# Optimization experiments

Hardware: AMD Instinct MI355X
Metric: run time of the kernel (lower is better)

Reference implementation:

```python
import jax, jax.numpy as jnp
import numpy as np

N_CLASSES = 4096
FEAT_DIM = 2048


def setup_inputs() -> dict:
    key = jax.random.key(0)
    k1, k2, k3 = jax.random.split(key, 3)
    boundaries = jax.random.uniform(k1, (N_CLASSES,), dtype=jnp.float32)
    prototypes = jax.random.normal(k2, (N_CLASSES, FEAT_DIM), dtype=jnp.float32)
    classifier_weights = jax.random.normal(k3, (N_CLASSES, FEAT_DIM), dtype=jnp.float32)
    return {"boundaries": boundaries, "prototypes": prototypes,
            "classifier_weights": classifier_weights}


def reference(boundaries, prototypes, classifier_weights):
    n = boundaries.shape[0]
    # L2-normalize prototypes along feature dim (F.normalize, eps=1e-12)
    norm = jnp.sqrt(jnp.sum(prototypes * prototypes, axis=-1, keepdims=True))
    p = prototypes / jnp.maximum(norm, 1e-12)
    # s[i, j] = <p_i, w_j>  -- one GEMM instead of N^2 tiny dots
    s = p @ classifier_weights.T  # [N, N]
    diag = jnp.diagonal(s)  # <p_i, w_i>, shape [N]
    # term1 depends only on i, term2 on (i, j)
    term1 = (1.0 - boundaries) * diag  # [N]
    term2 = s * (boundaries - 1.0)[None, :]  # [N, N], broadcast over j
    vals = jax.nn.relu(term1[:, None] + term2)  # [N, N]
    # exclude i == j
    off_diag_sum = jnp.sum(vals) - jnp.sum(jnp.diagonal(vals))
    return off_diag_sum / (n * (n - 1))
```

## Files before the change

kernel.cpp:

```cpp
#include <hip/hip_runtime.h>
#include <hip/hip_bf16.h>

#define N_CLS 4096
#define FDIM  2048
#define ITERS 8

typedef float  floatx4 __attribute__((ext_vector_type(4)));
typedef int    intx2   __attribute__((ext_vector_type(2)));
typedef int    intx4   __attribute__((ext_vector_type(4)));
typedef int    intx8   __attribute__((ext_vector_type(8)));

__global__ __launch_bounds__(256) void prep_kernel(
    const float* __restrict__ bnd,
    const float* __restrict__ proto,
    const float* __restrict__ wgt,
    unsigned char* __restrict__ pf8,
    unsigned char* __restrict__ wf8,
    float* __restrict__ t1,
    float* __restrict__ cc,
    float* __restrict__ accum)
{
    const int row = blockIdx.x;
    const int tid = threadIdx.x;
    const size_t base = (size_t)row * FDIM + (size_t)tid * 8;

    floatx4 p0 = *(const floatx4*)(proto + base);
    floatx4 p1 = *(const floatx4*)(proto + base + 4);
    floatx4 w0 = *(const floatx4*)(wgt + base);
    floatx4 w1 = *(const floatx4*)(wgt + base + 4);

    float ss = 0.f, dt = 0.f;
#pragma unroll
    for (int k = 0; k < 4; ++k) {
        ss += p0[k] * p0[k] + p1[k] * p1[k];
        dt += p0[k] * w0[k] + p1[k] * w1[k];
    }
#pragma unroll
    for (int off = 32; off > 0; off >>= 1) {
        ss += __shfl_down(ss, off);
        dt += __shfl_down(dt, off);
    }

    __shared__ float sss[4], sdt[4];
    __shared__ float srn;
    const int wid = tid >> 6, lane = tid & 63;
    if (lane == 0) { sss[wid] = ss; sdt[wid] = dt; }
    __syncthreads();
    if (tid == 0) {
        float SS = sss[0] + sss[1] + sss[2] + sss[3];
        float DT = sdt[0] + sdt[1] + sdt[2] + sdt[3];
        float rn = 1.0f / fmaxf(sqrtf(SS), 1e-12f);
        srn = rn;
        float bv = bnd[row];
        t1[row] = (1.0f - bv) * (DT * rn);
        cc[row] = bv - 1.0f;
        if (row == 0) *accum = 0.0f;
    }
    __syncthreads();
    const float rn = srn;

    intx2 pv, wv;
    {
        int a = __builtin_amdgcn_cvt_pk_fp8_f32(p0[0] * rn, p0[1] * rn, 0, 0);
        a     = __builtin_amdgcn_cvt_pk_fp8_f32(p0[2] * rn, p0[3] * rn, a, 1);
        int b = __builtin_amdgcn_cvt_pk_fp8_f32(p1[0] * rn, p1[1] * rn, 0, 0);
        b     = __builtin_amdgcn_cvt_pk_fp8_f32(p1[2] * rn, p1[3] * rn, b, 1);
        pv[0] = a; pv[1] = b;
        int c = __builtin_amdgcn_cvt_pk_fp8_f32(w0[0], w0[1], 0, 0);
        c     = __builtin_amdgcn_cvt_pk_fp8_f32(w0[2], w0[3], c, 1);
        int d = __builtin_amdgcn_cvt_pk_fp8_f32(w1[0], w1[1], 0, 0);
        d     = __builtin_amdgcn_cvt_pk_fp8_f32(w1[2], w1[3], d, 1);
        wv[0] = c; wv[1] = d;
    }
    *(intx2*)(pf8 + base) = pv;
    *(intx2*)(wf8 + base) = wv;
}

#define PH_BAR() { __builtin_amdgcn_s_barrier(); __builtin_amdgcn_sched_barrier(0); }
#define VMCNT(N) asm volatile("s_waitcnt vmcnt(" #N ")" ::: "memory")

#define RD_FA(D, MH)                                                           \
    _Pragma("unroll") for (int mi = 0; mi < 4; ++mi) {                         \
        const unsigned char* bp = &sAB[D][aoff + ((MH)*64 + mi*16) * 128];     \
        intx4* fp = (intx4*)&fa[mi];                                           \
        fp[0] = *(const intx4*)(bp + cq0);                                     \
        fp[1] = *(const intx4*)(bp + cq1);                                     \
    }
#define RD_FB2(D, NI0)                                                         \
    _Pragma("unroll") for (int ni = 0; ni < 2; ++ni) {                         \
        const unsigned char* bp = &sAB[D][boff + ((NI0)+ni) * 2048];           \
        intx4* fp = (intx4*)&fb[(NI0)+ni];                                     \
        fp[0] = *(const intx4*)(bp + cq0);                                     \
        fp[1] = *(const intx4*)(bp + cq1);                                     \
    }
#define MFMA_Q(MI0, NI0)                                                       \
    __builtin_amdgcn_s_setprio(1);                                             \
    _Pragma("unroll") for (int mi = 0; mi < 4; ++mi)                           \
    _Pragma("unroll") for (int ni = 0; ni < 2; ++ni)                           \
        acc[(MI0)+mi][(NI0)+ni] =                                              \
            __builtin_amdgcn_mfma_scale_f32_16x16x128_f8f6f4(                  \
                fa[mi], fb[(NI0)+ni], acc[(MI0)+mi][(NI0)+ni],                 \
                0, 0, 0, SC1, 0, SC1);                                         \
    __builtin_amdgcn_s_setprio(0);

__global__ __launch_bounds__(512, 1) void gemm_reduce_kernel(
    const unsigned char* __restrict__ A,
    const unsigned char* __restrict__ B,
    const float* __restrict__ t1,
    const float* __restrict__ cc,
    float* __restrict__ accum)
{
    __shared__ unsigned char sAB[2][65536];
    __shared__ float red[8];

    const int tid  = threadIdx.x;
    const int wid  = tid >> 6;
    const int lane = tid & 63;
    const int SC1  = 0x7F7F7F7F;

    const int b   = blockIdx.x;
    const int xcd = b & 7, sl = b >> 3;
    const int bi  = ((xcd & 3) << 2) + (sl & 3);
    const int bj  = ((xcd >> 2) << 3) + (sl >> 2);
    const int arow0 = bi * 256;
    const int brow0 = bj * 256;

    const int wm = wid >> 2;
    const int wn = wid & 3;
    const int lr = lane & 15;
    const int q  = lane >> 4;
    const int r7 = lane & 7;

    const int cq0 = ((q)     ^ r7) << 4;
    const int cq1 = ((4 | q) ^ r7) << 4;
    const int aoff = wm * 16384 + lr * 128;
    const int boff = 32768 + (wn >> 1) * 16384 + (wn & 1) * 8192 + lr * 128;

    const int srow = tid >> 3;
    const int sx   = (tid & 7) ^ ((tid >> 3) & 7);
    const int sgc  = (((sx & 3) << 1) | (sx >> 2)) << 4;

    auto glds = [&](const unsigned char* src, unsigned char* dst) {
        __builtin_amdgcn_global_load_lds(
            (const __attribute__((address_space(1))) void*)src,
            (__attribute__((address_space(3))) void*)dst, 16, 0, 0);
    };
    auto stageA = [&](int h, int t) {
        unsigned char* dst = &sAB[t & 1][h * 16384 + tid * 16];
        const unsigned char* src =
            A + (size_t)(arow0 + h * 128 + srow) * FDIM + t * 128 + sgc;
        glds(src, dst);
        glds(src + (size_t)64 * FDIM, dst + 8192);
    };
    auto stageB = [&](int h, int t) {
        unsigned char* dst = &sAB[t & 1][32768 + h * 16384 + tid * 16];
        const unsigned char* src =
            B + (size_t)(brow0 + h * 128 + srow) * FDIM + t * 128 + sgc;
        glds(src, dst);
        glds(src + (size_t)64 * FDIM, dst + 8192);
    };

    floatx4 acc[8][4];
#pragma unroll
    for (int m = 0; m < 8; ++m)
#pragma unroll
        for (int n = 0; n < 4; ++n) acc[m][n] = (floatx4)0.0f;

    intx8 fa[4];
    intx8 fb[4];

    stageB(0, 0); stageB(1, 0); stageA(0, 0); stageA(1, 0);
    stageB(0, 1); stageB(1, 1); stageA(0, 1);
    VMCNT(6);
    PH_BAR();

#pragma unroll 1
    for (int i = 0; i < ITERS - 1; ++i) {
        const int c2 = 2 * i + 2, c3 = 2 * i + 3;
        VMCNT(8);
        PH_BAR();
        RD_FA(0, 0); RD_FB2(0, 0);
        stageA(1, 2 * i + 1);
        MFMA_Q(0, 0);
        VMCNT(12);
        PH_BAR();
        RD_FB2(0, 2);
        stageB(0, c2);
        MFMA_Q(0, 2);
        VMCNT(10);
        PH_BAR();
        RD_FA(0, 1);
        stageB(1, c2);
        MFMA_Q(4, 2);
        PH_BAR();
        stageA(0, c2);
        MFMA_Q(4, 0);
        VMCNT(8);
        PH_BAR();
        RD_FA(1, 0); RD_FB2(1, 0);
        stageA(1, c2);
        MFMA_Q(0, 0);
        VMCNT(12);
        PH_BAR();
        RD_FB2(1, 2);
        stageB(0, c3);
        MFMA_Q(0, 2);
        VMCNT(10);
        PH_BAR();
        RD_FA(1, 1);
        stageB(1, c3);
        MFMA_Q(4, 2);
        PH_BAR();
        stageA(0, c3);
        MFMA_Q(4, 0);
    }

    {
        VMCNT(0);
        PH_BAR();
        RD_FA(0, 0); RD_FB2(0, 0);
        stageA(1, 15);
        MFMA_Q(0, 0);
        PH_BAR();
        RD_FB2(0, 2);
        MFMA_Q(0, 2);
        PH_BAR();
        RD_FA(0, 1);
        MFMA_Q(4, 2);
        PH_BAR();
        MFMA_Q(4, 0);
        PH_BAR();
        RD_FA(1, 0); RD_FB2(1, 0);
        MFMA_Q(0, 0);
        PH_BAR();
        RD_FB2(1, 2);
        MFMA_Q(0, 2);
        VMCNT(0);
        PH_BAR();
        RD_FA(1, 1);
        MFMA_Q(4, 2);
        PH_BAR();
        MFMA_Q(4, 0);
    }

    const int row0 = arow0 + wm * 128 + (lane >> 4) * 4;
    const int col0 = brow0 + wn * 64 + lr;

    float local = 0.f;
#pragma unroll
    for (int n = 0; n < 4; ++n) {
        const int j = col0 + n * 16;
        const float cj = cc[j];
#pragma unroll
        for (int m = 0; m < 8; ++m) {
#pragma unroll
            for (int r = 0; r < 4; ++r) {
                const int i = row0 + m * 16 + r;
                float v = fmaxf(t1[i] + acc[m][n][r] * cj, 0.f);
                local += (i == j) ? 0.f : v;
            }
        }
    }

#pragma unroll
    for (int off = 32; off > 0; off >>= 1)
        local += __shfl_down(local, off);
    if (lane == 0) red[wid] = local;
    __syncthreads();
    if (tid == 0) {
        float s = 0.f;
#pragma unroll
        for (int w = 0; w < 8; ++w) s += red[w];
        atomicAdd(accum, s);
    }
}

__global__ void finalize_kernel(const float* __restrict__ accum,
                                float* __restrict__ out)
{
    const float denom = 4096.0f * 4095.0f;
    out[0] = *accum / denom;
}

extern "C" void kernel_launch(void* const* d_in, const int* in_sizes, int n_in,
                              void* d_out, int out_size, void* d_ws, size_t ws_size,
                              hipStream_t stream) {
    const float* bnd   = (const float*)d_in[0];
    const float* proto = (const float*)d_in[1];
    const float* wgt   = (const float*)d_in[2];

    char* ws = (char*)d_ws;
    unsigned char* pf8 = (unsigned char*)ws;
    unsigned char* wf8 = (unsigned char*)(ws + (size_t)N_CLS * FDIM);
    float* t1    = (float*)(ws + (size_t)N_CLS * FDIM * 2);
    float* cc    = t1 + N_CLS;
    float* accum = cc + N_CLS;

    prep_kernel<<<N_CLS, 256, 0, stream>>>(bnd, proto, wgt, pf8, wf8, t1, cc, accum);
    gemm_reduce_kernel<<<256, 512, 0, stream>>>(pf8, wf8, t1, cc, accum);
    finalize_kernel<<<1, 1, 0, stream>>>(accum, (float*)d_out);
}
```

Before: 57.33 us.

## Replace fine-grained interleaved GEMM pipeline with simple double-buffered tile loop

Replaces the hand-scheduled, phase-interleaved main loop (partial waits on outstanding loads, prefetch spread across eight barrier phases) with a plain double-buffered loop. Each iteration waits for all loads, issues the full next tile's global-to-LDS copies, then does its fragment reads and MFMAs. This simplifies the schedule and cuts barriers per tile, but it waits on all outstanding loads (vmcnt 0) at every step and drops the fine-grained overlap. There is also only one barrier per iteration before restaging the other buffer, which may leave a race with waves still reading it.

```diff
diff --git a/kernel.cpp b/kernel.cpp
--- a/kernel.cpp
+++ b/kernel.cpp
@@ -3,7 +3,7 @@
 
 #define N_CLS 4096
 #define FDIM  2048
-#define ITERS 8
+#define NT    16
 
 typedef float  floatx4 __attribute__((ext_vector_type(4)));
 typedef int    intx2   __attribute__((ext_vector_type(2)));
@@ -169,78 +169,25 @@
     intx8 fa[4];
     intx8 fb[4];
 
-    stageB(0, 0); stageB(1, 0); stageA(0, 0); stageA(1, 0);
-    stageB(0, 1); stageB(1, 1); stageA(0, 1);
-    VMCNT(6);
-    PH_BAR();
+    stageA(0, 0); stageA(1, 0); stageB(0, 0); stageB(1, 0);
 
 #pragma unroll 1
-    for (int i = 0; i < ITERS - 1; ++i) {
-        const int c2 = 2 * i + 2, c3 = 2 * i + 3;
-        VMCNT(8);
-        PH_BAR();
-        RD_FA(0, 0); RD_FB2(0, 0);
-        stageA(1, 2 * i + 1);
-        MFMA_Q(0, 0);
-        VMCNT(12);
-        PH_BAR();
-        RD_FB2(0, 2);
-        stageB(0, c2);
-        MFMA_Q(0, 2);
-        VMCNT(10);
-        PH_BAR();
-        RD_FA(0, 1);
-        stageB(1, c2);
-        MFMA_Q(4, 2);
-        PH_BAR();
-        stageA(0, c2);
-        MFMA_Q(4, 0);
-        VMCNT(8);
-        PH_BAR();
-        RD_FA(1, 0); RD_FB2(1, 0);
-        stageA(1, c2);
-        MFMA_Q(0, 0);
-        VMCNT(12);
-        PH_BAR();
-        RD_FB2(1, 2);
-        stageB(0, c3);
-        MFMA_Q(0, 2);
-        VMCNT(10);
-        PH_BAR();
-        RD_FA(1, 1);
-        stageB(1, c3);
-        MFMA_Q(4, 2);
-        PH_BAR();
-        stageA(0, c3);
-        MFMA_Q(4, 0);
-    }
-
-    {
+    for (int t = 0; t < NT; ++t) {
+        const int D = t & 1;
+
         VMCNT(0);
         PH_BAR();
-        RD_FA(0, 0); RD_FB2(0, 0);
-        stageA(1, 15);
-        MFMA_Q(0, 0);
-        PH_BAR();
-        RD_FB2(0, 2);
-        MFMA_Q(0, 2);
-        PH_BAR();
-        RD_FA(0, 1);
-        MFMA_Q(4, 2);
-        PH_BAR();
-        MFMA_Q(4, 0);
-        PH_BAR();
-        RD_FA(1, 0); RD_FB2(1, 0);
-        MFMA_Q(0, 0);
-        PH_BAR();
-        RD_FB2(1, 2);
-        MFMA_Q(0, 2);
-        VMCNT(0);
-        PH_BAR();
-        RD_FA(1, 1);
-        MFMA_Q(4, 2);
-        PH_BAR();
-        MFMA_Q(4, 0);
+
+        if (t + 1 < NT) {
+            stageA(0, t + 1); stageA(1, t + 1);
+            stageB(0, t + 1); stageB(1, t + 1);
+        }
+
+        RD_FA(D, 0);
+        RD_FB2(D, 0); RD_FB2(D, 2);
+        MFMA_Q(0, 0); MFMA_Q(0, 2);
+        RD_FA(D, 1);
+        MFMA_Q(4, 0); MFMA_Q(4, 2);
     }
 
     const int row0 = arow0 + wm * 128 + (lane >> 4) * 4;
```

Result: faster. 53.42 us (median of 3 runs) (-6.8%).
